# Kernel optimization log

Measured on AMD Instinct MI355X. Metric: run time of the kernel, lower is better.

## Reference

```python
import jax, jax.numpy as jnp
import numpy as np

MARGIN = 0.1
EPS = 1e-6
NUM_COMPARE = 5
N, D = 32768, 512


def setup_inputs() -> dict:
    key = jax.random.key(0)
    k1, k2 = jax.random.split(key)
    output = jax.random.normal(k1, (N, D), dtype=jnp.float32)
    target = jax.random.normal(k2, (N, D), dtype=jnp.float32)
    return {"output": output, "target": target}


def reference(output, target):
    # torch CosineSimilarity(dim=0, eps=1e-6): dot(x,y) / max(||x||*||y||, eps)
    n = output.shape[0]
    on = jnp.linalg.norm(output, axis=-1)          # [N]
    tn = jnp.linalg.norm(target, axis=-1)          # [N]
    # positive similarity: cos(target[i], output[i])
    pos = jnp.sum(output * target, axis=-1) / jnp.maximum(on * tn, EPS)  # [N]
    # negative similarities: cos(target[j], output[i]) for j in 0..NUM_COMPARE-1
    t5 = target[:NUM_COMPARE]                      # [5, D]
    tn5 = tn[:NUM_COMPARE]                         # [5]
    S = (output @ t5.T) / jnp.maximum(on[:, None] * tn5[None, :], EPS)   # [N, 5]
    # mask out j == i (only affects first NUM_COMPARE rows)
    i_idx = jnp.arange(n)[:, None]
    j_idx = jnp.arange(NUM_COMPARE)[None, :]
    mask = (i_idx != j_idx).astype(output.dtype)   # [N, 5]
    hinge = jax.nn.relu(MARGIN - pos[:, None] + S) * mask
    count = n * NUM_COMPARE - min(n, NUM_COMPARE)  # pairs with j != i
    return jnp.sum(hinge) / count
```

## Files before the change

kernel.cpp:

```cpp
#include <hip/hip_runtime.h>


constexpr int D   = 512;
constexpr int NC  = 5;
constexpr float MARGIN_F = 0.1f;
constexpr float EPS_F    = 1e-6f;

__global__ __launch_bounds__(256) void hinge_dots_kernel(
    const float* __restrict__ out, const float* __restrict__ tgt,
    float* __restrict__ wave_partial, int n)
{
  const int tid  = threadIdx.x;
  const int wid  = tid >> 6;
  const int lane = tid & 63;
  const int sub  = lane & 15;
  const int grp  = lane >> 4;

  const float4* t5p = reinterpret_cast<const float4*>(tgt);

  float sq_own = 0.f, sq_4 = 0.f;
  #pragma unroll
  for (int c = 0; c < 8; ++c) {
    const float4 a = t5p[grp * 128 + c * 16 + sub];
    const float4 b = t5p[4   * 128 + c * 16 + sub];
    sq_own += a.x*a.x + a.y*a.y + a.z*a.z + a.w*a.w;
    sq_4   += b.x*b.x + b.y*b.y + b.z*b.z + b.w*b.w;
  }
  #pragma unroll
  for (int off = 8; off; off >>= 1) {
    sq_own += __shfl_xor(sq_own, off);
    sq_4   += __shfl_xor(sq_4,   off);
  }
  float tn5[NC];
  #pragma unroll
  for (int j = 0; j < 4; ++j) tn5[j] = sqrtf(__shfl(sq_own, j * 16 + sub));
  tn5[4] = sqrtf(sq_4);

  const int gwave = blockIdx.x * 4 + wid;
  const int row   = gwave * 4 + grp;
  float acc = 0.f;
  if (row < n) {
    const float4* op = reinterpret_cast<const float4*>(out) + (size_t)row * 128;
    const float4* tp = reinterpret_cast<const float4*>(tgt) + (size_t)row * 128;
    float s_ot = 0.f, s_oo = 0.f, s_tt = 0.f;
    float s5[NC] = {0.f, 0.f, 0.f, 0.f, 0.f};
    #pragma unroll
    for (int c = 0; c < 8; ++c) {
      const float4 o = op[c * 16 + sub];
      const float4 t = tp[c * 16 + sub];
      s_ot += o.x*t.x + o.y*t.y + o.z*t.z + o.w*t.w;
      s_oo += o.x*o.x + o.y*o.y + o.z*o.z + o.w*o.w;
      s_tt += t.x*t.x + t.y*t.y + t.z*t.z + t.w*t.w;
      #pragma unroll
      for (int j = 0; j < NC; ++j) {
        const float4 v = t5p[j * 128 + c * 16 + sub];
        s5[j] += o.x*v.x + o.y*v.y + o.z*v.z + o.w*v.w;
      }
    }
    #pragma unroll
    for (int off = 8; off; off >>= 1) {
      s_ot += __shfl_xor(s_ot, off);
      s_oo += __shfl_xor(s_oo, off);
      s_tt += __shfl_xor(s_tt, off);
      #pragma unroll
      for (int j = 0; j < NC; ++j) s5[j] += __shfl_xor(s5[j], off);
    }
    const float on  = sqrtf(s_oo);
    const float tn  = sqrtf(s_tt);
    const float pos = s_ot / fmaxf(on * tn, EPS_F);
    float h = 0.f;
    #pragma unroll
    for (int j = 0; j < NC; ++j) {
      const float S = s5[j] / fmaxf(on * tn5[j], EPS_F);
      const float hv = fmaxf(0.f, MARGIN_F - pos + S);
      h += (row == j) ? 0.f : hv;
    }
    acc = (sub == 0) ? h : 0.f;
  }
  acc += __shfl_xor(acc, 16);
  acc += __shfl_xor(acc, 32);
  if (lane == 0) wave_partial[gwave] = acc;
}

__global__ __launch_bounds__(256) void reduce_kernel(
    const float* __restrict__ part, float* __restrict__ result,
    int nw, float inv_count)
{
  float s = 0.f;
  for (int i = threadIdx.x; i < nw; i += 256) s += part[i];
  #pragma unroll
  for (int off = 32; off; off >>= 1) s += __shfl_xor(s, off);
  __shared__ float ws[4];
  if ((threadIdx.x & 63) == 0) ws[threadIdx.x >> 6] = s;
  __syncthreads();
  if (threadIdx.x == 0) result[0] = (ws[0] + ws[1] + ws[2] + ws[3]) * inv_count;
}

extern "C" void kernel_launch(void* const* d_in, const int* in_sizes, int n_in,
                              void* d_out, int out_size, void* d_ws, size_t ws_size,
                              hipStream_t stream) {
  const float* out = (const float*)d_in[0];
  const float* tgt = (const float*)d_in[1];
  float* result = (float*)d_out;
  float* partials = (float*)d_ws;

  const int n = in_sizes[0] / D;
  const int blocks = (n + 15) / 16;
  const int nwaves = blocks * 4;
  const long long count = (long long)n * NC - (n < NC ? n : NC);
  const float inv_count = 1.0f / (float)count;

  hinge_dots_kernel<<<blocks, 256, 0, stream>>>(out, tgt, partials, n);
  reduce_kernel<<<1, 256, 0, stream>>>(partials, result, nwaves, inv_count);
}
```

Before: 154.4 us.

## Hold target[0:5] in registers and process four rows per wave in full

Each wave now loads the five comparison target rows into registers once and reuses them across four rows. Each of those four rows is spread over all 64 lanes. Previously each 16-lane group streamed its own row and reloaded the t5 slices from cache on every chunk. This cuts repeated t5 loads and issues all row loads up front to raise memory-level parallelism. In exchange it needs many more registers and a 6-step, 4-row shuffle reduction with 32 values per step, which may lower occupancy.

```diff
diff --git a/kernel.cpp b/kernel.cpp
--- a/kernel.cpp
+++ b/kernel.cpp
@@ -6,6 +6,10 @@
 constexpr float MARGIN_F = 0.1f;
 constexpr float EPS_F    = 1e-6f;
 
+__device__ __forceinline__ float dot4(const float4 a, const float4 b) {
+  return a.x*b.x + a.y*b.y + a.z*b.z + a.w*b.w;
+}
+
 __global__ __launch_bounds__(256) void hinge_dots_kernel(
     const float* __restrict__ out, const float* __restrict__ tgt,
     float* __restrict__ wave_partial, int n)
@@ -13,73 +17,83 @@
   const int tid  = threadIdx.x;
   const int wid  = tid >> 6;
   const int lane = tid & 63;
-  const int sub  = lane & 15;
-  const int grp  = lane >> 4;
 
   const float4* t5p = reinterpret_cast<const float4*>(tgt);
 
-  float sq_own = 0.f, sq_4 = 0.f;
+  float4 t5r[NC][2];
   #pragma unroll
-  for (int c = 0; c < 8; ++c) {
-    const float4 a = t5p[grp * 128 + c * 16 + sub];
-    const float4 b = t5p[4   * 128 + c * 16 + sub];
-    sq_own += a.x*a.x + a.y*a.y + a.z*a.z + a.w*a.w;
-    sq_4   += b.x*b.x + b.y*b.y + b.z*b.z + b.w*b.w;
+  for (int j = 0; j < NC; ++j) {
+    t5r[j][0] = t5p[j * 128 + lane];
+    t5r[j][1] = t5p[j * 128 + 64 + lane];
   }
+
+  float tsq[NC];
   #pragma unroll
-  for (int off = 8; off; off >>= 1) {
-    sq_own += __shfl_xor(sq_own, off);
-    sq_4   += __shfl_xor(sq_4,   off);
+  for (int j = 0; j < NC; ++j)
+    tsq[j] = dot4(t5r[j][0], t5r[j][0]) + dot4(t5r[j][1], t5r[j][1]);
+  #pragma unroll
+  for (int off = 32; off; off >>= 1) {
+    #pragma unroll
+    for (int j = 0; j < NC; ++j) tsq[j] += __shfl_xor(tsq[j], off);
   }
   float tn5[NC];
   #pragma unroll
-  for (int j = 0; j < 4; ++j) tn5[j] = sqrtf(__shfl(sq_own, j * 16 + sub));
-  tn5[4] = sqrtf(sq_4);
+  for (int j = 0; j < NC; ++j) tn5[j] = sqrtf(tsq[j]);
 
   const int gwave = blockIdx.x * 4 + wid;
-  const int row   = gwave * 4 + grp;
-  float acc = 0.f;
-  if (row < n) {
-    const float4* op = reinterpret_cast<const float4*>(out) + (size_t)row * 128;
-    const float4* tp = reinterpret_cast<const float4*>(tgt) + (size_t)row * 128;
-    float s_ot = 0.f, s_oo = 0.f, s_tt = 0.f;
-    float s5[NC] = {0.f, 0.f, 0.f, 0.f, 0.f};
+  const int row0  = gwave * 4;
+  float4 o[4][2], t[4][2];
+  #pragma unroll
+  for (int r = 0; r < 4; ++r) {
+    const size_t rr = (size_t)min(row0 + r, n - 1) * 128;
+    const float4* op = reinterpret_cast<const float4*>(out) + rr;
+    const float4* tp = reinterpret_cast<const float4*>(tgt) + rr;
+    o[r][0] = op[lane];  o[r][1] = op[64 + lane];
+    t[r][0] = tp[lane];  t[r][1] = tp[64 + lane];
+  }
+
+  float s_ot[4], s_oo[4], s_tt[4], s5[4][NC];
+  #pragma unroll
+  for (int r = 0; r < 4; ++r) {
+    s_ot[r] = dot4(o[r][0], t[r][0]) + dot4(o[r][1], t[r][1]);
+    s_oo[r] = dot4(o[r][0], o[r][0]) + dot4(o[r][1], o[r][1]);
+    s_tt[r] = dot4(t[r][0], t[r][0]) + dot4(t[r][1], t[r][1]);
     #pragma unroll
-    for (int c = 0; c < 8; ++c) {
-      const float4 o = op[c * 16 + sub];
-      const float4 t = tp[c * 16 + sub];
-      s_ot += o.x*t.x + o.y*t.y + o.z*t.z + o.w*t.w;
-      s_oo += o.x*o.x + o.y*o.y + o.z*o.z + o.w*o.w;
-      s_tt += t.x*t.x + t.y*t.y + t.z*t.z + t.w*t.w;
+    for (int j = 0; j < NC; ++j)
+      s5[r][j] = dot4(o[r][0], t5r[j][0]) + dot4(o[r][1], t5r[j][1]);
+  }
+
+  #pragma unroll
+  for (int off = 32; off; off >>= 1) {
+    #pragma unroll
+    for (int r = 0; r < 4; ++r) {
+      s_ot[r] += __shfl_xor(s_ot[r], off);
+      s_oo[r] += __shfl_xor(s_oo[r], off);
+      s_tt[r] += __shfl_xor(s_tt[r], off);
       #pragma unroll
-      for (int j = 0; j < NC; ++j) {
-        const float4 v = t5p[j * 128 + c * 16 + sub];
-        s5[j] += o.x*v.x + o.y*v.y + o.z*v.z + o.w*v.w;
+      for (int j = 0; j < NC; ++j) s5[r][j] += __shfl_xor(s5[r][j], off);
+    }
+  }
+
+  if (lane == 0) {
+    float acc = 0.f;
+    #pragma unroll
+    for (int r = 0; r < 4; ++r) {
+      const int row = row0 + r;
+      if (row < n) {
+        const float on  = sqrtf(s_oo[r]);
+        const float tn  = sqrtf(s_tt[r]);
+        const float pos = s_ot[r] / fmaxf(on * tn, EPS_F);
+        #pragma unroll
+        for (int j = 0; j < NC; ++j) {
+          const float S = s5[r][j] / fmaxf(on * tn5[j], EPS_F);
+          const float h = fmaxf(0.f, MARGIN_F - pos + S);
+          acc += (row == j) ? 0.f : h;
+        }
       }
     }
-    #pragma unroll
-    for (int off = 8; off; off >>= 1) {
-      s_ot += __shfl_xor(s_ot, off);
-      s_oo += __shfl_xor(s_oo, off);
-      s_tt += __shfl_xor(s_tt, off);
-      #pragma unroll
-      for (int j = 0; j < NC; ++j) s5[j] += __shfl_xor(s5[j], off);
-    }
-    const float on  = sqrtf(s_oo);
-    const float tn  = sqrtf(s_tt);
-    const float pos = s_ot / fmaxf(on * tn, EPS_F);
-    float h = 0.f;
-    #pragma unroll
-    for (int j = 0; j < NC; ++j) {
-      const float S = s5[j] / fmaxf(on * tn5[j], EPS_F);
-      const float hv = fmaxf(0.f, MARGIN_F - pos + S);
-      h += (row == j) ? 0.f : hv;
-    }
-    acc = (sub == 0) ? h : 0.f;
+    wave_partial[gwave] = acc;
   }
-  acc += __shfl_xor(acc, 16);
-  acc += __shfl_xor(acc, 32);
-  if (lane == 0) wave_partial[gwave] = acc;
 }
 
 __global__ __launch_bounds__(256) void reduce_kernel(
```

After: 159.2 us. +3.1%, slower.

## Map one wave per row, precompute target norms, use DPP reductions

Applied to the files above, without the earlier changes.

Rows are now assigned one per 64-lane wave instead of four rows per wave with 16 lanes each. Each lane loads two float4s per row, which raises memory-level parallelism and makes the block count four times larger. The norms of the first five target rows move into a separate one-block kernel, so each wave no longer recomputes them. Wave reductions now use DPP row operations before cross-row shuffles. The cost is an extra kernel launch and more reduction work per row, since every row now reduces over 64 lanes instead of 16.

```diff
diff --git a/kernel.cpp b/kernel.cpp
--- a/kernel.cpp
+++ b/kernel.cpp
@@ -6,80 +6,87 @@
 constexpr float MARGIN_F = 0.1f;
 constexpr float EPS_F    = 1e-6f;
 
-__global__ __launch_bounds__(256) void hinge_dots_kernel(
+__device__ __forceinline__ float dot4(const float4 a, const float4 b) {
+  return a.x*b.x + a.y*b.y + a.z*b.z + a.w*b.w;
+}
+
+template <int CTRL>
+__device__ __forceinline__ float dpp_add(float x) {
+  const int y = __builtin_amdgcn_update_dpp(
+      0, __float_as_int(x), CTRL, 0xF, 0xF, true);
+  return x + __int_as_float(y);
+}
+
+__device__ __forceinline__ float red64(float x) {
+  x = dpp_add<0xB1>(x);
+  x = dpp_add<0x4E>(x);
+  x = dpp_add<0x124>(x);
+  x = dpp_add<0x128>(x);
+  x += __shfl_xor(x, 16);
+  x += __shfl_xor(x, 32);
+  return x;
+}
+
+__global__ __launch_bounds__(320) void tn5_kernel(
+    const float* __restrict__ tgt, float* __restrict__ tn5_out)
+{
+  const int w = threadIdx.x >> 6, lane = threadIdx.x & 63;
+  const float4* tp = reinterpret_cast<const float4*>(tgt) + w * 128;
+  const float4 a = tp[lane], b = tp[64 + lane];
+  const float s = red64(dot4(a, a) + dot4(b, b));
+  if (lane == 0) tn5_out[w] = sqrtf(s);
+}
+
+__global__ __launch_bounds__(256) void hinge_kernel(
     const float* __restrict__ out, const float* __restrict__ tgt,
-    float* __restrict__ wave_partial, int n)
+    const float* __restrict__ tn5g, float* __restrict__ partial, int n)
 {
   const int tid  = threadIdx.x;
   const int wid  = tid >> 6;
   const int lane = tid & 63;
-  const int sub  = lane & 15;
-  const int grp  = lane >> 4;
+  const int row  = blockIdx.x * 4 + wid;
+  __shared__ float bsum[4];
 
-  const float4* t5p = reinterpret_cast<const float4*>(tgt);
-
-  float sq_own = 0.f, sq_4 = 0.f;
-  #pragma unroll
-  for (int c = 0; c < 8; ++c) {
-    const float4 a = t5p[grp * 128 + c * 16 + sub];
-    const float4 b = t5p[4   * 128 + c * 16 + sub];
-    sq_own += a.x*a.x + a.y*a.y + a.z*a.z + a.w*a.w;
-    sq_4   += b.x*b.x + b.y*b.y + b.z*b.z + b.w*b.w;
-  }
-  #pragma unroll
-  for (int off = 8; off; off >>= 1) {
-    sq_own += __shfl_xor(sq_own, off);
-    sq_4   += __shfl_xor(sq_4,   off);
-  }
-  float tn5[NC];
-  #pragma unroll
-  for (int j = 0; j < 4; ++j) tn5[j] = sqrtf(__shfl(sq_own, j * 16 + sub));
-  tn5[4] = sqrtf(sq_4);
-
-  const int gwave = blockIdx.x * 4 + wid;
-  const int row   = gwave * 4 + grp;
-  float acc = 0.f;
+  float h = 0.f;
   if (row < n) {
     const float4* op = reinterpret_cast<const float4*>(out) + (size_t)row * 128;
     const float4* tp = reinterpret_cast<const float4*>(tgt) + (size_t)row * 128;
-    float s_ot = 0.f, s_oo = 0.f, s_tt = 0.f;
-    float s5[NC] = {0.f, 0.f, 0.f, 0.f, 0.f};
+    const float4 o0 = op[lane], o1 = op[64 + lane];
+    const float4 t0 = tp[lane], t1 = tp[64 + lane];
+
+    const float4* t5p = reinterpret_cast<const float4*>(tgt);
+    float s_ot = dot4(o0, t0) + dot4(o1, t1);
+    float s_oo = dot4(o0, o0) + dot4(o1, o1);
+    float s_tt = dot4(t0, t0) + dot4(t1, t1);
+    float s5[NC];
     #pragma unroll
-    for (int c = 0; c < 8; ++c) {
-      const float4 o = op[c * 16 + sub];
-      const float4 t = tp[c * 16 + sub];
-      s_ot += o.x*t.x + o.y*t.y + o.z*t.z + o.w*t.w;
-      s_oo += o.x*o.x + o.y*o.y + o.z*o.z + o.w*o.w;
-      s_tt += t.x*t.x + t.y*t.y + t.z*t.z + t.w*t.w;
+    for (int j = 0; j < NC; ++j) {
+      const float4 v0 = t5p[j * 128 + lane];
+      const float4 v1 = t5p[j * 128 + 64 + lane];
+      s5[j] = dot4(o0, v0) + dot4(o1, v1);
+    }
+
+    s_ot = red64(s_ot);
+    s_oo = red64(s_oo);
+    s_tt = red64(s_tt);
+    #pragma unroll
+    for (int j = 0; j < NC; ++j) s5[j] = red64(s5[j]);
+
+    if (lane == 0) {
+      const float on  = sqrtf(s_oo);
+      const float tn  = sqrtf(s_tt);
+      const float pos = s_ot / fmaxf(on * tn, EPS_F);
       #pragma unroll
       for (int j = 0; j < NC; ++j) {
-        const float4 v = t5p[j * 128 + c * 16 + sub];
-        s5[j] += o.x*v.x + o.y*v.y + o.z*v.z + o.w*v.w;
+        const float S = s5[j] / fmaxf(on * tn5g[j], EPS_F);
+        const float hv = fmaxf(0.f, MARGIN_F - pos + S);
+        h += (row == j) ? 0.f : hv;
       }
     }
-    #pragma unroll
-    for (int off = 8; off; off >>= 1) {
-      s_ot += __shfl_xor(s_ot, off);
-      s_oo += __shfl_xor(s_oo, off);
-      s_tt += __shfl_xor(s_tt, off);
-      #pragma unroll
-      for (int j = 0; j < NC; ++j) s5[j] += __shfl_xor(s5[j], off);
-    }
-    const float on  = sqrtf(s_oo);
-    const float tn  = sqrtf(s_tt);
-    const float pos = s_ot / fmaxf(on * tn, EPS_F);
-    float h = 0.f;
-    #pragma unroll
-    for (int j = 0; j < NC; ++j) {
-      const float S = s5[j] / fmaxf(on * tn5[j], EPS_F);
-      const float hv = fmaxf(0.f, MARGIN_F - pos + S);
-      h += (row == j) ? 0.f : hv;
-    }
-    acc = (sub == 0) ? h : 0.f;
   }
-  acc += __shfl_xor(acc, 16);
-  acc += __shfl_xor(acc, 32);
-  if (lane == 0) wave_partial[gwave] = acc;
+  if (lane == 0) bsum[wid] = h;
+  __syncthreads();
+  if (tid == 0) partial[blockIdx.x] = bsum[0] + bsum[1] + bsum[2] + bsum[3];
 }
 
 __global__ __launch_bounds__(256) void reduce_kernel(
@@ -88,8 +95,7 @@
 {
   float s = 0.f;
   for (int i = threadIdx.x; i < nw; i += 256) s += part[i];
-  #pragma unroll
-  for (int off = 32; off; off >>= 1) s += __shfl_xor(s, off);
+  s = red64(s);
   __shared__ float ws[4];
   if ((threadIdx.x & 63) == 0) ws[threadIdx.x >> 6] = s;
   __syncthreads();
@@ -101,15 +107,16 @@
                               hipStream_t stream) {
   const float* out = (const float*)d_in[0];
   const float* tgt = (const float*)d_in[1];
-  float* result = (float*)d_out;
+  float* result   = (float*)d_out;
   float* partials = (float*)d_ws;
+  float* tn5_ws   = partials + 8192;
 
   const int n = in_sizes[0] / D;
-  const int blocks = (n + 15) / 16;
-  const int nwaves = blocks * 4;
+  const int blocks = (n + 3) / 4;
   const long long count = (long long)n * NC - (n < NC ? n : NC);
   const float inv_count = 1.0f / (float)count;
 
-  hinge_dots_kernel<<<blocks, 256, 0, stream>>>(out, tgt, partials, n);
-  reduce_kernel<<<1, 256, 0, stream>>>(partials, result, nwaves, inv_count);
+  tn5_kernel<<<1, 320, 0, stream>>>(tgt, tn5_ws);
+  hinge_kernel<<<blocks, 256, 0, stream>>>(out, tgt, tn5_ws, partials, n);
+  reduce_kernel<<<1, 256, 0, stream>>>(partials, result, blocks, inv_count);
 }
```

After: 148.6 us. -3.7%, faster.
